# Optimization experiments

Hardware: AMD Instinct MI355X
Metric: run time of the kernel (lower is better)

The kernel has to match this reference:

```python
import jax, jax.numpy as jnp
import numpy as np

GAMMA = 0.9  # decay (init kwarg)


def setup_inputs() -> dict:
    key = jax.random.key(0)
    k0, k1, k2, k3 = jax.random.split(key, 4)
    B, T, D = 16, 2048, 256
    x = jax.random.normal(k0, (B, T, D), jnp.float32)
    scale = 1.0 / np.sqrt(D)
    Wq = jax.random.normal(k1, (D, D), jnp.float32) * scale
    Wk = jax.random.normal(k2, (D, D), jnp.float32) * scale
    Wv = jax.random.normal(k3, (D, D), jnp.float32) * scale
    return {"x": x, "Wq": Wq, "Wk": Wk, "Wv": Wv}


def reference(x, Wq, Wk, Wv):
    # x: [B, T, D]
    B, T, D = x.shape
    Q = x @ Wq  # [B, T, D]
    K = x @ Wk
    V = x @ Wv

    # Sequential retention recurrence over the [D, D] state:
    #   s[t] = gamma * s[t-1] + K[:, t, :]^T @ V[:, t, :]   (sums over batch, as in source)
    Kt = jnp.swapaxes(K, 0, 1)  # [T, B, D]
    Vt = jnp.swapaxes(V, 0, 1)  # [T, B, D]

    def step(s, kv):
        k_t, v_t = kv  # each [B, D]
        s = GAMMA * s + k_t.T @ v_t  # [D, D]
        return s, s.sum(-1)  # emit row-sum [D]

    # Loop runs t = 1 .. T-1 in the source (s starts at 0); s[0] := s[1].
    init = jnp.zeros((D, D), x.dtype)
    _, rows = jax.lax.scan(step, init, (Kt[1:], Vt[1:]))  # rows: [T-1, D]
    S = jnp.concatenate([rows[:1], rows], axis=0)  # [T, D]

    # Faithful to tf.reshape(S, [-1, seq_len]) then tf.transpose: a reshape-scramble,
    # NOT a plain transpose of S.
    S2 = S.reshape(D, T).T  # [T, D]
    return S2[None, :, :] * Q  # broadcast over batch -> [B, T, D]
```

## Files before the change

### kernel.cpp

```cpp
#include <hip/hip_runtime.h>
#include <math.h>


#define GAMMA_F 0.9f
#define T_LEN 2048
#define D_DIM 256
#define B_DIM 16

typedef __attribute__((ext_vector_type(8))) short bf16x8;
typedef __attribute__((ext_vector_type(16))) float f32x16;

__device__ inline ushort f2bf(float f) {
    union { float f; unsigned u; } v; v.f = f;
    unsigned r = (v.u + 0x7FFFu + ((v.u >> 16) & 1u)) >> 16;
    return (ushort)r;
}

__device__ __forceinline__ void gload_lds16(const void* g, void* l) {
    __builtin_amdgcn_global_load_lds(
        (const __attribute__((address_space(1))) unsigned int*)g,
        (__attribute__((address_space(3))) unsigned int*)l, 16, 0, 0);
}

__global__ __launch_bounds__(256) void k_prep(const float* __restrict__ Wq,
                                              const float* __restrict__ Wk,
                                              const float* __restrict__ Wv,
                                              ushort* __restrict__ WqT,
                                              ushort* __restrict__ WkT,
                                              float* __restrict__ wv_sum) {
    int bid = blockIdx.x;
    int tid = threadIdx.x;
    if (bid < 32) {
        __shared__ float tile[64][68];
        const float* W = (bid < 16) ? Wq : Wk;
        ushort* WT = (bid < 16) ? WqT : WkT;
        int b = bid & 15;
        int k0 = (b & 3) * 64;
        int n0 = (b >> 2) * 64;
        int r = tid >> 4;
        int c4 = (tid & 15) * 4;
#pragma unroll
        for (int i = 0; i < 4; ++i) {
            float4 v = *(const float4*)(W + (size_t)(k0 + r + 16 * i) * D_DIM + n0 + c4);
            *(float4*)&tile[r + 16 * i][c4] = v;
        }
        __syncthreads();
        int n = tid >> 2;
        int j0 = (tid & 3) * 16;
        ushort tmp[16];
#pragma unroll
        for (int i = 0; i < 16; ++i) tmp[i] = f2bf(tile[j0 + i][n]);
        ushort* dst = WT + (size_t)(n0 + n) * D_DIM + k0 + j0;
#pragma unroll
        for (int i = 0; i < 16; ++i) dst[i] = tmp[i];
    } else {
        int j = (bid - 32) * 64 + (tid >> 2);
        int q = tid & 3;
        const float4* row4 = (const float4*)(Wv + (size_t)j * D_DIM + q * 64);
        float s = 0.f;
#pragma unroll
        for (int i = 0; i < 16; ++i) {
            float4 v = row4[i];
            s += v.x + v.y + v.z + v.w;
        }
        s += __shfl_xor(s, 1, 64);
        s += __shfl_xor(s, 2, 64);
        if (q == 0) wv_sum[j] = s;
    }
}

__global__ __launch_bounds__(256) void k_y(const float* __restrict__ x,
                                           const float* __restrict__ wv_sum,
                                           ushort* __restrict__ ybf,
                                           ushort* __restrict__ xbf) {
    int tid = threadIdx.x;
    int lane = tid & 63;
    int t = blockIdx.x * 4 + (tid >> 6);
    int d0 = lane * 4;
    float4 wv4 = *(const float4*)(wv_sum + d0);

    float4 xr[B_DIM];
    float w[B_DIM];
#pragma unroll
    for (int b = 0; b < B_DIM; ++b) {
        xr[b] = *(const float4*)(x + ((size_t)b * T_LEN + t) * D_DIM + d0);
        float p = xr[b].x * wv4.x + xr[b].y * wv4.y + xr[b].z * wv4.z + xr[b].w * wv4.w;
#pragma unroll
        for (int o = 32; o > 0; o >>= 1) p += __shfl_xor(p, o, 64);
        w[b] = p;
    }

    float4 acc = make_float4(0.f, 0.f, 0.f, 0.f);
#pragma unroll
    for (int b = 0; b < B_DIM; ++b) {
        acc.x += w[b] * xr[b].x;
        acc.y += w[b] * xr[b].y;
        acc.z += w[b] * xr[b].z;
        acc.w += w[b] * xr[b].w;
        ushort4 s;
        s.x = f2bf(xr[b].x); s.y = f2bf(xr[b].y);
        s.z = f2bf(xr[b].z); s.w = f2bf(xr[b].w);
        *(ushort4*)&xbf[((size_t)b * T_LEN + t) * D_DIM + d0] = s;
    }
    ushort4 ys;
    ys.x = f2bf(acc.x); ys.y = f2bf(acc.y);
    ys.z = f2bf(acc.z); ys.w = f2bf(acc.w);
    *(ushort4*)&ybf[(size_t)t * D_DIM + d0] = ys;
}

__global__ __launch_bounds__(256) void k_gs(const ushort* __restrict__ ybf,
                                            const ushort* __restrict__ WkT,
                                            float* __restrict__ loc,
                                            float* __restrict__ carry) {
    __shared__ ushort As[32 * 64 * 8];
    __shared__ ushort Bs[32 * 64 * 8];
    float* Cs = (float*)As;
    int mt = blockIdx.x >> 2;
    int nt = blockIdx.x & 3;
    int tid = threadIdx.x, lane = tid & 63, w = tid >> 6;
    int wr = w >> 1, wc = w & 1, l31 = lane & 31, lh = lane >> 5;

#pragma unroll
    for (int i = 0; i < 8; ++i) {
        int slot = tid + 256 * i;
        int r = slot >> 5;
        int s2h = slot & 31;
        int rs = r ^ (s2h & 7);
        *(bf16x8*)&As[(s2h * 64 + rs) * 8] =
            *(const bf16x8*)&ybf[(size_t)(mt * 64 + r) * D_DIM + s2h * 8];
        *(bf16x8*)&Bs[(s2h * 64 + rs) * 8] =
            *(const bf16x8*)&WkT[(size_t)(nt * 64 + r) * D_DIM + s2h * 8];
    }
    __syncthreads();

    f32x16 acc;
#pragma unroll
    for (int e = 0; e < 16; ++e) acc[e] = 0.f;
#pragma unroll
    for (int s = 0; s < 16; ++s) {
        int s2h = s * 2 + lh;
        int ra = (wr * 32 + l31) ^ (s2h & 7);
        int rb = (wc * 32 + l31) ^ (s2h & 7);
        bf16x8 a = *(bf16x8*)&As[(s2h * 64 + ra) * 8];
        bf16x8 b = *(bf16x8*)&Bs[(s2h * 64 + rb) * 8];
        acc = __builtin_amdgcn_mfma_f32_32x32x16_bf16(a, b, acc, 0, 0, 0);
    }
    __syncthreads();

#pragma unroll
    for (int reg = 0; reg < 16; ++reg) {
        int rr = (reg & 3) + 8 * (reg >> 2) + 4 * lh;
        Cs[(wr * 32 + rr) * 64 + wc * 32 + l31] = acc[reg];
    }
    __syncthreads();

#pragma unroll
    for (int half = 0; half < 2; ++half) {
        int task = half * 256 + tid;
        int dl = task & 63;
        int cl = task >> 6;
        float a = 0.f;
#pragma unroll
        for (int j = 0; j < 8; ++j) {
            int tl = cl * 8 + j;
            int gt = mt * 64 + tl;
            float v = (gt == 0) ? 0.f : Cs[tl * 64 + dl];
            a = GAMMA_F * a + v;
            loc[(size_t)gt * D_DIM + nt * 64 + dl] = a;
        }
        carry[(size_t)(mt * 8 + cl) * D_DIM + nt * 64 + dl] = a;
    }
}

__global__ __launch_bounds__(256) void k_qgemm(const ushort* __restrict__ xbf,
                                               const ushort* __restrict__ WqT,
                                               const float* __restrict__ loc,
                                               const float* __restrict__ carry,
                                               float* __restrict__ out) {
    __shared__ char QL[65536] __attribute__((aligned(128)));
    int bid = blockIdx.x;
    int mb = bid >> 1;
    int nb = bid & 1;
    int tid = threadIdx.x;
    int lane = tid & 63, w = tid >> 6;
    int wr = w >> 1, wc = w & 1;
    int l31 = lane & 31, lh = lane >> 5;

    f32x16 acc[2][2];
#pragma unroll
    for (int i = 0; i < 2; ++i)
#pragma unroll
        for (int j = 0; j < 2; ++j)
#pragma unroll
            for (int e = 0; e < 16; ++e) acc[i][j][e] = 0.f;

    const ushort* ab = xbf + (size_t)mb * 128 * D_DIM;
    const ushort* bb = WqT + (size_t)nb * 128 * D_DIM;

#define ASP(buf) ((ushort*)(QL + (buf) * 16384))
#define BSP(buf) ((ushort*)(QL + 32768 + (buf) * 16384))
#define STAGE(buf, kb)                                                        \
    do {                                                                      \
        _Pragma("unroll")                                                     \
        for (int i = 0; i < 4; ++i) {                                         \
            int slot = i * 256 + tid;             \
            int kk = slot >> 7;                                               \
            int row = slot & 127;                                             \
            int ldsbase = (i * 256 + w * 64) * 8;      \
            gload_lds16(ab + (size_t)row * D_DIM + (kb) * 64 + kk * 8,        \
                        ASP(buf) + ldsbase);                                  \
            gload_lds16(bb + (size_t)row * D_DIM + (kb) * 64 + kk * 8,        \
                        BSP(buf) + ldsbase);                                  \
        }                                                                     \
    } while (0)

    STAGE(0, 0);
    __syncthreads();

#pragma unroll
    for (int kb = 0; kb < 4; ++kb) {
        int cur = kb & 1;
        if (kb < 3) STAGE(cur ^ 1, kb + 1);
#pragma unroll
        for (int s = 0; s < 4; ++s) {
            int c0 = (s * 2 + lh) * 128;
            bf16x8 a0 = *(bf16x8*)&ASP(cur)[(c0 + wr * 64 + l31) * 8];
            bf16x8 a1 = *(bf16x8*)&ASP(cur)[(c0 + wr * 64 + 32 + l31) * 8];
            bf16x8 b0 = *(bf16x8*)&BSP(cur)[(c0 + wc * 64 + l31) * 8];
            bf16x8 b1 = *(bf16x8*)&BSP(cur)[(c0 + wc * 64 + 32 + l31) * 8];
            acc[0][0] = __builtin_amdgcn_mfma_f32_32x32x16_bf16(a0, b0, acc[0][0], 0, 0, 0);
            acc[0][1] = __builtin_amdgcn_mfma_f32_32x32x16_bf16(a0, b1, acc[0][1], 0, 0, 0);
            acc[1][0] = __builtin_amdgcn_mfma_f32_32x32x16_bf16(a1, b0, acc[1][0], 0, 0, 0);
            acc[1][1] = __builtin_amdgcn_mfma_f32_32x32x16_bf16(a1, b1, acc[1][1], 0, 0, 0);
        }
        if (kb < 3) __syncthreads();
    }
#undef STAGE
#undef ASP
#undef BSP

    __syncthreads();

    float* Ls = (float*)QL;
    {
        int rloc = tid & 127;
        int h = tid >> 7;
        int rglob = (mb & 1) * 128 + rloc;
        int o = (mb & 15) >> 1;
        int gn0 = nb * 128;
        int gstart = gn0 + h * 64;
        const float g8 = 0.43046721f;
        const float log2g = -0.15200309344504995f;
        float gpo = exp2f((float)(o + 1) * log2g);

        float p = 0.f;
        if (gstart > 0) {
            float wgt = 1.f;
#pragma unroll
            for (int i = 1; i <= 32; ++i) {
                p += wgt * carry[(size_t)(gstart - i) * D_DIM + rglob];
                wgt *= g8;
            }
        }
#pragma unroll 8
        for (int gl = 0; gl < 64; ++gl) {
            int gn = gstart + gl;
            float locv = loc[(size_t)(8 * gn + o) * D_DIM + rglob];
            float Av = fmaf(gpo, p, locv);
            if (o == 0 && gn == 0) Av = loc[D_DIM + rglob];
            int gnl = gn - gn0;
            Ls[rloc * 128 + (gnl ^ (rloc & 31))] = Av;
            p = p * g8 + carry[(size_t)gn * D_DIM + rglob];
        }
    }
    __syncthreads();

    size_t row_base = (size_t)mb * 128;
#pragma unroll
    for (int mi = 0; mi < 2; ++mi) {
#pragma unroll
        for (int ni = 0; ni < 2; ++ni) {
            int gnl = wc * 64 + ni * 32 + l31;
            int gn_out = nb * 128 + gnl;
#pragma unroll
            for (int reg = 0; reg < 16; ++reg) {
                int rr = (reg & 3) + 8 * (reg >> 2) + 4 * lh;
                int m = wr * 64 + mi * 32 + rr;
                float av = Ls[m * 128 + (gnl ^ (m & 31))];
                out[(row_base + m) * D_DIM + gn_out] = acc[mi][ni][reg] * av;
            }
        }
    }
}

extern "C" void kernel_launch(void* const* d_in, const int* in_sizes, int n_in,
                              void* d_out, int out_size, void* d_ws, size_t ws_size,
                              hipStream_t stream) {
    const float* x  = (const float*)d_in[0];
    const float* Wq = (const float*)d_in[1];
    const float* Wk = (const float*)d_in[2];
    const float* Wv = (const float*)d_in[3];
    float* out = (float*)d_out;

    float* ws = (float*)d_ws;
    float* loc    = ws;
    float* wv_sum = ws + 1048576 + 256 - 256;
    wv_sum = ws + 1048576;
    float* carry  = wv_sum + 256;
    ushort* WqT   = (ushort*)(carry + 65536);
    ushort* WkT   = WqT + 65536;
    ushort* ybf   = WkT + 65536;
    ushort* xbf   = ybf + 524288;

    k_prep<<<36, 256, 0, stream>>>(Wq, Wk, Wv, WqT, WkT, wv_sum);
    k_y<<<T_LEN / 4, 256, 0, stream>>>(x, wv_sum, ybf, xbf);
    k_gs<<<128, 256, 0, stream>>>(ybf, WkT, loc, carry);
    k_qgemm<<<(B_DIM * T_LEN / 128) * 2, 256, 0, stream>>>(xbf, WqT, loc, carry, out);
}
```

Baseline: 116.1 us.

## Split batch across waves in k_y and remap block IDs for XCD locality

k_y now handles each timestep with two waves, each covering half the batch, and combines the partial sums through shared memory. This halves per-thread register pressure and doubles the grid size to improve memory-level parallelism. k_gs and k_qgemm remap blockIdx so that consecutive tiles land on the same XCD (stride-8 interleave), aiming at better L2 reuse. The cost is one extra __syncthreads and an LDS round trip in k_y.

```diff
diff --git a/kernel.cpp b/kernel.cpp
--- a/kernel.cpp
+++ b/kernel.cpp
@@ -73,39 +73,49 @@
                                            const float* __restrict__ wv_sum,
                                            ushort* __restrict__ ybf,
                                            ushort* __restrict__ xbf) {
+    __shared__ float4 part[4][64];
     int tid = threadIdx.x;
-    int lane = tid & 63;
-    int t = blockIdx.x * 4 + (tid >> 6);
+    int lane = tid & 63, wave = tid >> 6;
+    int t = blockIdx.x * 2 + (wave >> 1);
+    int bh = wave & 1;
     int d0 = lane * 4;
     float4 wv4 = *(const float4*)(wv_sum + d0);
 
-    float4 xr[B_DIM];
-    float w[B_DIM];
-#pragma unroll
-    for (int b = 0; b < B_DIM; ++b) {
-        xr[b] = *(const float4*)(x + ((size_t)b * T_LEN + t) * D_DIM + d0);
-        float p = xr[b].x * wv4.x + xr[b].y * wv4.y + xr[b].z * wv4.z + xr[b].w * wv4.w;
+    float4 xr[8];
+    float w[8];
+#pragma unroll
+    for (int i = 0; i < 8; ++i) {
+        int b = bh * 8 + i;
+        xr[i] = *(const float4*)(x + ((size_t)b * T_LEN + t) * D_DIM + d0);
+        float p = xr[i].x * wv4.x + xr[i].y * wv4.y + xr[i].z * wv4.z + xr[i].w * wv4.w;
 #pragma unroll
         for (int o = 32; o > 0; o >>= 1) p += __shfl_xor(p, o, 64);
-        w[b] = p;
+        w[i] = p;
     }
 
     float4 acc = make_float4(0.f, 0.f, 0.f, 0.f);
 #pragma unroll
-    for (int b = 0; b < B_DIM; ++b) {
-        acc.x += w[b] * xr[b].x;
-        acc.y += w[b] * xr[b].y;
-        acc.z += w[b] * xr[b].z;
-        acc.w += w[b] * xr[b].w;
+    for (int i = 0; i < 8; ++i) {
+        int b = bh * 8 + i;
+        acc.x += w[i] * xr[i].x;
+        acc.y += w[i] * xr[i].y;
+        acc.z += w[i] * xr[i].z;
+        acc.w += w[i] * xr[i].w;
         ushort4 s;
-        s.x = f2bf(xr[b].x); s.y = f2bf(xr[b].y);
-        s.z = f2bf(xr[b].z); s.w = f2bf(xr[b].w);
+        s.x = f2bf(xr[i].x); s.y = f2bf(xr[i].y);
+        s.z = f2bf(xr[i].z); s.w = f2bf(xr[i].w);
         *(ushort4*)&xbf[((size_t)b * T_LEN + t) * D_DIM + d0] = s;
     }
-    ushort4 ys;
-    ys.x = f2bf(acc.x); ys.y = f2bf(acc.y);
-    ys.z = f2bf(acc.z); ys.w = f2bf(acc.w);
-    *(ushort4*)&ybf[(size_t)t * D_DIM + d0] = ys;
+    part[wave][lane] = acc;
+    __syncthreads();
+    if (bh == 0) {
+        float4 other = part[wave ^ 1][lane];
+        acc.x += other.x; acc.y += other.y; acc.z += other.z; acc.w += other.w;
+        ushort4 ys;
+        ys.x = f2bf(acc.x); ys.y = f2bf(acc.y);
+        ys.z = f2bf(acc.z); ys.w = f2bf(acc.w);
+        *(ushort4*)&ybf[(size_t)t * D_DIM + d0] = ys;
+    }
 }
 
 __global__ __launch_bounds__(256) void k_gs(const ushort* __restrict__ ybf,
@@ -115,8 +125,10 @@
     __shared__ ushort As[32 * 64 * 8];
     __shared__ ushort Bs[32 * 64 * 8];
     float* Cs = (float*)As;
-    int mt = blockIdx.x >> 2;
-    int nt = blockIdx.x & 3;
+    int bid = blockIdx.x;
+    int v = (bid & 7) * 16 + (bid >> 3);
+    int mt = v >> 2;
+    int nt = v & 3;
     int tid = threadIdx.x, lane = tid & 63, w = tid >> 6;
     int wr = w >> 1, wc = w & 1, l31 = lane & 31, lh = lane >> 5;
 
@@ -164,8 +176,8 @@
         for (int j = 0; j < 8; ++j) {
             int tl = cl * 8 + j;
             int gt = mt * 64 + tl;
-            float v = (gt == 0) ? 0.f : Cs[tl * 64 + dl];
-            a = GAMMA_F * a + v;
+            float v2 = (gt == 0) ? 0.f : Cs[tl * 64 + dl];
+            a = GAMMA_F * a + v2;
             loc[(size_t)gt * D_DIM + nt * 64 + dl] = a;
         }
         carry[(size_t)(mt * 8 + cl) * D_DIM + nt * 64 + dl] = a;
@@ -179,8 +191,9 @@
                                                float* __restrict__ out) {
     __shared__ char QL[65536] __attribute__((aligned(128)));
     int bid = blockIdx.x;
-    int mb = bid >> 1;
-    int nb = bid & 1;
+    int v = (bid & 7) * 64 + (bid >> 3);
+    int mb = v >> 1;
+    int nb = v & 1;
     int tid = threadIdx.x;
     int lane = tid & 63, w = tid >> 6;
     int wr = w >> 1, wc = w & 1;
@@ -304,8 +317,7 @@
 
     float* ws = (float*)d_ws;
     float* loc    = ws;
-    float* wv_sum = ws + 1048576 + 256 - 256;
-    wv_sum = ws + 1048576;
+    float* wv_sum = ws + 1048576;
     float* carry  = wv_sum + 256;
     ushort* WqT   = (ushort*)(carry + 65536);
     ushort* WkT   = WqT + 65536;
@@ -313,7 +325,7 @@
     ushort* xbf   = ybf + 524288;
 
     k_prep<<<36, 256, 0, stream>>>(Wq, Wk, Wv, WqT, WkT, wv_sum);
-    k_y<<<T_LEN / 4, 256, 0, stream>>>(x, wv_sum, ybf, xbf);
+    k_y<<<T_LEN / 2, 256, 0, stream>>>(x, wv_sum, ybf, xbf);
     k_gs<<<128, 256, 0, stream>>>(ybf, WkT, loc, carry);
     k_qgemm<<<(B_DIM * T_LEN / 128) * 2, 256, 0, stream>>>(xbf, WqT, loc, carry, out);
 }
```

Measured after the change: 116.8 us. No clear change (+0.6%).
